# Performance work log

Hardware: AMD Instinct MI355X
Metric: run time of the kernel (lower is better)

## Reference

```python
import jax, jax.numpy as jnp
import numpy as np

EPS = 1e-12  # matches torch F.normalize eps


def setup_inputs() -> dict:
    key = jax.random.key(0)
    k1, k2 = jax.random.split(key)
    N, D, K = 262144, 128, 512
    embeddings = jax.random.normal(k1, (N, D), dtype=jnp.float32)
    init_centroids = jax.random.normal(k2, (K, D), dtype=jnp.float32)
    return {"embeddings": embeddings, "init_centroids": init_centroids, "num_iters": 5}


def _kmeans_iter(centroids, embeddings, K):
    # [N, K] similarity, hard assignment by argmax (k-means E-step with dot-product metric)
    dots = jnp.matmul(embeddings, centroids.T)
    assign = jnp.argmax(dots, axis=1)  # [N] int32
    # M-step: per-cluster sum + counts (replaces CPU dict-of-lists + python loop)
    emb_sums = jax.ops.segment_sum(embeddings, assign, num_segments=K)  # [K, D]
    counts = jax.ops.segment_sum(jnp.ones(embeddings.shape[0], dtype=embeddings.dtype),
                                 assign, num_segments=K)  # [K]
    # only update clusters with members (mask = counts > 0), keep old centroid otherwise
    new_c = jnp.where(counts[:, None] > 0,
                      emb_sums / jnp.maximum(counts, 1.0)[:, None],
                      centroids)
    # F.normalize(dim=1, p=2) applied to ALL centroids
    norm = jnp.maximum(jnp.linalg.norm(new_c, axis=1, keepdims=True), EPS)
    return new_c / norm, assign


def reference(embeddings, init_centroids, num_iters):
    K = init_centroids.shape[0]
    centroids = init_centroids
    assign = jnp.zeros(embeddings.shape[0], dtype=jnp.int32)
    for _ in range(num_iters):  # small static iteration count (k-means iters)
        centroids, assign = _kmeans_iter(centroids, embeddings, K)
    return assign, centroids
```

## Files before the change

### kernel.cpp

```cpp
#include <hip/hip_runtime.h>

#define NN 262144
#define DD 128
#define KK 512
#define NITER 5

#define SKH 136

#define SE 132
#define SC 260
#define SS 129

#define DELTA 2e-3f

#define WS_A16_BYTES   (NN * 2)
#define WS_SUMS_OFF    (WS_A16_BYTES)
#define WS_CNTS_OFF    (WS_SUMS_OFF + 2048 * DD * 4)
#define WS_NEEDED      (WS_CNTS_OFF + 2048 * 4)
#define WS_CH_OFF      (WS_SUMS_OFF + NN)
#define WS_CL_OFF      (WS_CH_OFF + KK * DD * 2)
#define WS_EAB3_OFF    (WS_NEEDED)
#define WS_EAB3_BYTES  (NN * DD * 4)
#define WS_NEEDED2     (WS_EAB3_OFF + WS_EAB3_BYTES)

using s8     = __attribute__((ext_vector_type(8))) short;
using f32x4  = __attribute__((ext_vector_type(4))) float;
using f32x16 = __attribute__((ext_vector_type(16))) float;

__device__ __forceinline__ unsigned f2bf(float x) {
    unsigned u = __float_as_uint(x);
    return (u + 0x7fffu + ((u >> 16) & 1u)) >> 16;
}

__device__ __forceinline__ void split4(float4 v, uint2& h, uint2& s) {
    unsigned hx = f2bf(v.x), hy = f2bf(v.y), hz = f2bf(v.z), hw = f2bf(v.w);
    float rx = v.x - __uint_as_float(hx << 16);
    float ry = v.y - __uint_as_float(hy << 16);
    float rz = v.z - __uint_as_float(hz << 16);
    float rw = v.w - __uint_as_float(hw << 16);
    unsigned lx = f2bf(rx), ly = f2bf(ry), lz = f2bf(rz), lw = f2bf(rw);
    h.x = hx | (hy << 16); h.y = hz | (hw << 16);
    s.x = lx | (ly << 16); s.y = lz | (lw << 16);
}

__global__ __launch_bounds__(256) void presplit_e3_kernel(
    const float* __restrict__ E, unsigned short* __restrict__ EAB)
{
    const int u   = blockIdx.x * 4 + (threadIdx.x >> 6);
    const int l   = threadIdx.x & 63;
    const int g32 = u >> 3, ks = u & 7;
    const int row = g32 * 32 + (l & 31);
    const int k0  = ks * 16 + (l >> 5) * 8;
    float4 v0 = *(const float4*)&E[(size_t)row * DD + k0];
    float4 v1 = *(const float4*)&E[(size_t)row * DD + k0 + 4];
    uint2 h0, s0, h1, s1;
    split4(v0, h0, s0); split4(v1, h1, s1);
    size_t base = (size_t)u * 2048 + l * 16;
    *(uint2*)((char*)EAB + base)        = h0;
    *(uint2*)((char*)EAB + base + 8)    = h1;
    *(uint2*)((char*)EAB + base + 1024) = s0;
    *(uint2*)((char*)EAB + base + 1032) = s1;
}

__global__ __launch_bounds__(256) void split_c3_kernel(
    const float* __restrict__ C, unsigned short* __restrict__ CH,
    unsigned short* __restrict__ CL)
{
    int idx = blockIdx.x * 256 + threadIdx.x;
    int col = idx >> 5;
    int k4  = (idx & 31) << 2;
    float4 v = *(const float4*)&C[(size_t)col * DD + k4];
    uint2 h, s;
    split4(v, h, s);
    int unit = (col >> 5) * 8 + (k4 >> 4);
    int lane = (col & 31) + ((k4 >> 3) & 1) * 32;
    int off  = unit * 512 + lane * 8 + (k4 & 7);
    *(uint2*)&CH[off] = h;
    *(uint2*)&CL[off] = s;
}

__global__ __launch_bounds__(256, 2) void assign4_kernel(
    const unsigned short* __restrict__ EAB,
    const unsigned short* __restrict__ CH, const unsigned short* __restrict__ CL,
    int* __restrict__ assignv, unsigned short* __restrict__ assign16,
    unsigned char* __restrict__ flags)
{
    const int tid = threadIdx.x;
    const int l   = tid & 63;
    const int wid = tid >> 6;
    const int j   = l & 31;
    const int h   = l >> 5;
    const int r0  = blockIdx.x * 128;
    const int g32 = blockIdx.x * 4 + wid;

    const char* Abase = (const char*)EAB + (size_t)g32 * 16384 + l * 16;
    s8 Ah[8], Al[8];
#pragma unroll
    for (int ks = 0; ks < 8; ++ks) {
        Ah[ks] = *(const s8*)(Abase + ks * 2048);
        Al[ks] = *(const s8*)(Abase + ks * 2048 + 1024);
    }

    float bv[16], sv[16];
    int   bk[16];
#pragma unroll
    for (int i = 0; i < 16; ++i) { bv[i] = -3.4e38f; sv[i] = -3.4e38f; bk[i] = 0; }

    const int boff0 = l * 8;

    s8 bh[2][4], bl[2][4];
#pragma unroll
    for (int cf = 0; cf < 4; ++cf) {
        bh[0][cf] = *(const s8*)&CH[(cf * 8) * 512 + boff0];
        bl[0][cf] = *(const s8*)&CL[(cf * 8) * 512 + boff0];
    }

    f32x16 acc[4];

#pragma unroll
    for (int t = 0; t < 32; ++t) {
        const int cc  = t >> 3, ks = t & 7;
        const int cur = t & 1,  nxt = cur ^ 1;

        if (ks == 0) {
#pragma unroll
            for (int cf = 0; cf < 4; ++cf)
#pragma unroll
                for (int r = 0; r < 16; ++r) acc[cf][r] = 0.f;
        }

        if (t < 31) {
            const int t1 = t + 1, cc1 = t1 >> 3, ks1 = t1 & 7;
#pragma unroll
            for (int cf = 0; cf < 4; ++cf) {
                const int unit = (cc1 * 4 + cf) * 8 + ks1;
                bh[nxt][cf] = *(const s8*)&CH[unit * 512 + boff0];
                bl[nxt][cf] = *(const s8*)&CL[unit * 512 + boff0];
            }
        }

#pragma unroll
        for (int cf = 0; cf < 4; ++cf) {
            acc[cf] = __builtin_amdgcn_mfma_f32_32x32x16_bf16(
                Ah[ks], bh[cur][cf], acc[cf], 0, 0, 0);
            acc[cf] = __builtin_amdgcn_mfma_f32_32x32x16_bf16(
                Ah[ks], bl[cur][cf], acc[cf], 0, 0, 0);
            acc[cf] = __builtin_amdgcn_mfma_f32_32x32x16_bf16(
                Al[ks], bh[cur][cf], acc[cf], 0, 0, 0);
        }

        if (ks == 7) {
#pragma unroll
            for (int cf = 0; cf < 4; ++cf) {
                const int kg = cc * 128 + cf * 32 + j;
#pragma unroll
                for (int r = 0; r < 16; ++r) {
                    float v = acc[cf][r];
                    if (v > bv[r]) { sv[r] = bv[r]; bv[r] = v; bk[r] = kg; }
                    else           { sv[r] = fmaxf(sv[r], v); }
                }
            }
        }
    }

#pragma unroll
    for (int r = 0; r < 16; ++r) {
        float v1 = bv[r], v2 = sv[r]; int k1 = bk[r];
#pragma unroll
        for (int m = 1; m <= 16; m <<= 1) {
            float ov = __shfl_xor(v1, m, 64);
            float os = __shfl_xor(v2, m, 64);
            int   ok = __shfl_xor(k1, m, 64);
            if (ov > v1) { v2 = fmaxf(v1, os); v1 = ov; k1 = ok; }
            else         { v2 = fmaxf(v2, ov); }
        }
        bv[r] = v1; sv[r] = v2; bk[r] = k1;
    }

#pragma unroll
    for (int r = 0; r < 16; ++r) {
        if (j == r) {
            int rowg = r0 + wid * 32 + (r & 3) + 8 * (r >> 2) + 4 * h;
            assignv[rowg]  = bk[r];
            assign16[rowg] = (unsigned short)bk[r];
            flags[rowg]    = (bv[r] - sv[r] < DELTA) ? 1 : 0;
        }
    }
}

__global__ __launch_bounds__(256) void split_c_kernel(
    const float* __restrict__ C, unsigned short* __restrict__ CH,
    unsigned short* __restrict__ CL)
{
    int idx = blockIdx.x * 256 + threadIdx.x;
    int col = idx >> 5;
    int k4  = (idx & 31) << 2;
    float4 v = *(const float4*)&C[(size_t)col * DD + k4];
    uint2 h, s;
    split4(v, h, s);
    int group = (col >> 4) * 4 + (k4 >> 5);
    int inner = ((k4 >> 3) & 3) * 16 + (col & 15);
    int off   = group * 512 + inner * 8 + (k4 & 7);
    *(uint2*)&CH[off] = h;
    *(uint2*)&CL[off] = s;
}

__global__ __launch_bounds__(256, 2) void assign_kernel(
    const float* __restrict__ E,
    const unsigned short* __restrict__ CH, const unsigned short* __restrict__ CL,
    int* __restrict__ assignv, unsigned short* __restrict__ assign16,
    unsigned char* __restrict__ flags)
{
    __shared__ unsigned short lds[2 * 128 * SKH];
    unsigned short* EH = lds;
    unsigned short* EL = lds + 128 * SKH;

    const int tid = threadIdx.x;
    const int l   = tid & 63;
    const int wid = tid >> 6;
    const int wr  = wid >> 1;
    const int wc  = wid & 1;
    const int c   = l & 15;
    const int g   = l >> 4;
    const int r0  = blockIdx.x * 128;

#pragma unroll
    for (int it = 0; it < 16; ++it) {
        int idx = it * 256 + tid;
        int row = idx >> 5;
        int k4  = (idx & 31) << 2;
        float4 v = *(const float4*)&E[(size_t)(r0 + row) * DD + k4];
        uint2 h, s;
        split4(v, h, s);
        *(uint2*)&EH[row * SKH + k4] = h;
        *(uint2*)&EL[row * SKH + k4] = s;
    }
    __syncthreads();

    float bv[16], sv[16];
    int   bk[16];
#pragma unroll
    for (int i = 0; i < 16; ++i) { bv[i] = -3.4e38f; sv[i] = -3.4e38f; bk[i] = 0; }

    const int aoff0 = (wr * 64 + c) * SKH + g * 8;
    const int bbase = wc * 16 * 512 + l * 8;

    s8 bh[2][4], bl[2][4];
#pragma unroll
    for (int cf = 0; cf < 4; ++cf) {
        int off = bbase + (cf * 4) * 512;
        bh[0][cf] = *(const s8*)&CH[off];
        bl[0][cf] = *(const s8*)&CL[off];
    }

    f32x4 acc[4][4];

#pragma unroll
    for (int t = 0; t < 16; ++t) {
        const int cc  = t >> 2, kc = t & 3;
        const int cur = t & 1,  nxt = cur ^ 1;

        if (kc == 0) {
#pragma unroll
            for (int rf = 0; rf < 4; ++rf)
#pragma unroll
                for (int cf = 0; cf < 4; ++cf)
                    acc[rf][cf] = (f32x4){0.f, 0.f, 0.f, 0.f};
        }

        if (t < 15) {
            const int t1 = t + 1, cc1 = t1 >> 2, kc1 = t1 & 3;
#pragma unroll
            for (int cf = 0; cf < 4; ++cf) {
                int off = bbase + (cc1 * 32 + cf * 4 + kc1) * 512;
                bh[nxt][cf] = *(const s8*)&CH[off];
                bl[nxt][cf] = *(const s8*)&CL[off];
            }
        }

        s8 ah[4], al[4];
#pragma unroll
        for (int rf = 0; rf < 4; ++rf) {
            int off = aoff0 + rf * 16 * SKH + kc * 32;
            ah[rf] = *(const s8*)&EH[off];
            al[rf] = *(const s8*)&EL[off];
        }

#pragma unroll
        for (int rf = 0; rf < 4; ++rf)
#pragma unroll
            for (int cf = 0; cf < 4; ++cf) {
                acc[rf][cf] = __builtin_amdgcn_mfma_f32_16x16x32_bf16(
                    ah[rf], bh[cur][cf], acc[rf][cf], 0, 0, 0);
                acc[rf][cf] = __builtin_amdgcn_mfma_f32_16x16x32_bf16(
                    ah[rf], bl[cur][cf], acc[rf][cf], 0, 0, 0);
                acc[rf][cf] = __builtin_amdgcn_mfma_f32_16x16x32_bf16(
                    al[rf], bh[cur][cf], acc[rf][cf], 0, 0, 0);
            }

        if (kc == 3) {
            const int kbase = cc * 128 + wc * 64 + c;
#pragma unroll
            for (int rf = 0; rf < 4; ++rf)
#pragma unroll
                for (int i = 0; i < 4; ++i) {
                    const int sidx = rf * 4 + i;
#pragma unroll
                    for (int cf = 0; cf < 4; ++cf) {
                        float v = acc[rf][cf][i];
                        int  kg = kbase + cf * 16;
                        if (v > bv[sidx]) { sv[sidx] = bv[sidx]; bv[sidx] = v; bk[sidx] = kg; }
                        else              { sv[sidx] = fmaxf(sv[sidx], v); }
                    }
                }
        }
    }

#pragma unroll
    for (int s = 0; s < 16; ++s) {
        float v1 = bv[s], v2 = sv[s]; int k1 = bk[s];
#pragma unroll
        for (int m = 1; m <= 8; m <<= 1) {
            float ov = __shfl_xor(v1, m, 64);
            float os = __shfl_xor(v2, m, 64);
            int   ok = __shfl_xor(k1, m, 64);
            if (ov > v1) { v2 = fmaxf(v1, os); v1 = ov; k1 = ok; }
            else         { v2 = fmaxf(v2, ov); }
        }
        bv[s] = v1; sv[s] = v2; bk[s] = k1;
    }

    __syncthreads();
    float* mv = (float*)lds;
    int*   mk = (int*)lds + 256;
    float* ms = (float*)lds + 512;
    if (c == 0) {
#pragma unroll
        for (int rf = 0; rf < 4; ++rf)
#pragma unroll
            for (int i = 0; i < 4; ++i) {
                int row = wr * 64 + rf * 16 + g * 4 + i;
                mv[wc * 128 + row] = bv[rf * 4 + i];
                mk[wc * 128 + row] = bk[rf * 4 + i];
                ms[wc * 128 + row] = sv[rf * 4 + i];
            }
    }
    __syncthreads();
    if (tid < 128) {
        float v1 = mv[tid], v2 = ms[tid]; int k1 = mk[tid];
        float ov = mv[128 + tid], os = ms[128 + tid]; int ok = mk[128 + tid];
        if (ov > v1) { v2 = fmaxf(v1, os); v1 = ov; k1 = ok; }
        else         { v2 = fmaxf(v2, ov); }
        assignv[r0 + tid] = k1;
        assign16[r0 + tid] = (unsigned short)k1;
        flags[r0 + tid] = (v1 - v2 < DELTA) ? 1 : 0;
    }
}

__global__ __launch_bounds__(256) void rescue_kernel(
    const float* __restrict__ E, const float* __restrict__ C,
    const unsigned char* __restrict__ flags,
    int* __restrict__ assignv, unsigned short* __restrict__ assign16)
{
    __shared__ int   rows[128];
    __shared__ int   nf;
    __shared__ float ev[DD];
    __shared__ float rv[4];
    __shared__ int   rk[4];

    const int tid  = threadIdx.x;
    const int base = blockIdx.x * 128;

    if (tid == 0) nf = 0;
    __syncthreads();
    if (tid < 128 && flags[base + tid]) {
        int p = atomicAdd(&nf, 1);
        rows[p] = base + tid;
    }
    __syncthreads();
    const int n = nf;
    if (n == 0) return;

    for (int i = 0; i < n; ++i) {
        const int row = rows[i];
        if (tid < 32)
            *(float4*)&ev[tid * 4] = *(const float4*)&E[(size_t)row * DD + tid * 4];
        __syncthreads();

        float d0 = 0.f, d1 = 0.f;
        for (int q = 0; q < 32; ++q) {
            float4 e4 = *(const float4*)&ev[q * 4];
            float4 c0 = *(const float4*)&C[(size_t)tid * DD + q * 4];
            float4 c1 = *(const float4*)&C[(size_t)(tid + 256) * DD + q * 4];
            d0 = fmaf(e4.x, c0.x, d0); d0 = fmaf(e4.y, c0.y, d0);
            d0 = fmaf(e4.z, c0.z, d0); d0 = fmaf(e4.w, c0.w, d0);
            d1 = fmaf(e4.x, c1.x, d1); d1 = fmaf(e4.y, c1.y, d1);
            d1 = fmaf(e4.z, c1.z, d1); d1 = fmaf(e4.w, c1.w, d1);
        }
        float v = (d0 >= d1) ? d0 : d1;
        int   k = (d0 >= d1) ? tid : tid + 256;
#pragma unroll
        for (int m = 1; m <= 32; m <<= 1) {
            float ov = __shfl_xor(v, m, 64);
            int   ok = __shfl_xor(k, m, 64);
            if (ov > v || (ov == v && ok < k)) { v = ov; k = ok; }
        }
        if ((tid & 63) == 0) { rv[tid >> 6] = v; rk[tid >> 6] = k; }
        __syncthreads();
        if (tid == 0) {
            float bv2 = rv[0]; int bk2 = rk[0];
#pragma unroll
            for (int w = 1; w < 4; ++w)
                if (rv[w] > bv2 || (rv[w] == bv2 && rk[w] < bk2)) { bv2 = rv[w]; bk2 = rk[w]; }
            assignv[row] = bk2;
            assign16[row] = (unsigned short)bk2;
        }
        __syncthreads();
    }
}

__global__ __launch_bounds__(256, 2) void assign_valu_kernel(
    const float* __restrict__ E, const float* __restrict__ C,
    int* __restrict__ assignv, unsigned short* __restrict__ assign16)
{
    __shared__ float smem[32 * SE + 32 * SC];
    float* ET = smem;
    float* CT = smem + 32 * SE;
    float* sval = smem;
    int*   sidx = ((int*)smem) + 32 * SS;

    const int tid = threadIdx.x;
    const int tx  = tid & 31;
    const int ty  = tid >> 5;
    const int r0  = blockIdx.x * 128;

    float bbv = 0.f;
    int   bbk = 0;

    for (int chunk = 0; chunk < 2; ++chunk) {
        const int k0 = chunk * 256;
        float acc[16][8];
#pragma unroll
        for (int i = 0; i < 16; ++i)
#pragma unroll
            for (int j = 0; j < 8; ++j) acc[i][j] = 0.f;

        for (int sub = 0; sub < 4; ++sub) {
            const int d0 = sub * 32;
            __syncthreads();
#pragma unroll
            for (int it = 0; it < 4; ++it) {
                int idx = tid + it * 256;
                int r = idx >> 3, q = idx & 7;
                float4 v = *(const float4*)&E[(r0 + r) * DD + d0 + q * 4];
                ET[(q * 4 + 0) * SE + r] = v.x;
                ET[(q * 4 + 1) * SE + r] = v.y;
                ET[(q * 4 + 2) * SE + r] = v.z;
                ET[(q * 4 + 3) * SE + r] = v.w;
            }
#pragma unroll
            for (int it = 0; it < 8; ++it) {
                int idx = tid + it * 256;
                int k = idx >> 3, q = idx & 7;
                float4 v = *(const float4*)&C[(k0 + k) * DD + d0 + q * 4];
                CT[(q * 4 + 0) * SC + k] = v.x;
                CT[(q * 4 + 1) * SC + k] = v.y;
                CT[(q * 4 + 2) * SC + k] = v.z;
                CT[(q * 4 + 3) * SC + k] = v.w;
            }
            __syncthreads();
#pragma unroll 4
            for (int d = 0; d < 32; ++d) {
                float4 a0 = *(const float4*)&ET[d * SE + ty * 16];
                float4 a1 = *(const float4*)&ET[d * SE + ty * 16 + 4];
                float4 a2 = *(const float4*)&ET[d * SE + ty * 16 + 8];
                float4 a3 = *(const float4*)&ET[d * SE + ty * 16 + 12];
                float4 b0 = *(const float4*)&CT[d * SC + tx * 4];
                float4 b1 = *(const float4*)&CT[d * SC + 128 + tx * 4];
                float ra[16] = {a0.x, a0.y, a0.z, a0.w, a1.x, a1.y, a1.z, a1.w,
                                a2.x, a2.y, a2.z, a2.w, a3.x, a3.y, a3.z, a3.w};
                float rb[8]  = {b0.x, b0.y, b0.z, b0.w, b1.x, b1.y, b1.z, b1.w};
#pragma unroll
                for (int i = 0; i < 16; ++i)
#pragma unroll
                    for (int j = 0; j < 8; ++j)
                        acc[i][j] = fmaf(ra[i], rb[j], acc[i][j]);
            }
        }
        __syncthreads();

#pragma unroll
        for (int i = 0; i < 16; ++i) {
            float bv = acc[i][0]; int bj = 0;
#pragma unroll
            for (int j = 1; j < 8; ++j)
                if (acc[i][j] > bv) { bv = acc[i][j]; bj = j; }
            int row = ty * 16 + i;
            int gk = k0 + ((bj < 4) ? (tx * 4 + bj) : (128 + tx * 4 + (bj - 4)));
            sval[tx * SS + row] = bv;
            sidx[tx * SS + row] = gk;
        }
        __syncthreads();
        if (tid < 128) {
            float bv = sval[tid]; int bi = sidx[tid];
            for (int t = 1; t < 32; ++t) {
                float v = sval[t * SS + tid];
                int   x = sidx[t * SS + tid];
                if (v > bv || (v == bv && x < bi)) { bv = v; bi = x; }
            }
            if (chunk == 0 || bv > bbv || (bv == bbv && bi < bbk)) {
                bbv = bv; bbk = bi;
            }
        }
    }
    if (tid < 128) {
        assignv[r0 + tid] = bbk;
        if (assign16) assign16[r0 + tid] = (unsigned short)bbk;
    }
}

__global__ __launch_bounds__(256) void update_partial_kernel(
    const float* __restrict__ E, const unsigned short* __restrict__ assign16,
    float* __restrict__ ws_sums, int* __restrict__ ws_cnts)
{
    const int b   = blockIdx.x;
    const int k   = b >> 2;
    const int qtr = b & 3;

    __shared__ float acc[4][DD];
    __shared__ int   cnts[4];

    const int tid  = threadIdx.x;
    const int w    = tid >> 6;
    const int lane = tid & 63;

    float a0 = 0.f, a1 = 0.f;
    int cnt = 0;
    const int wbase = qtr * (NN / 4) + w * (NN / 16);

    for (int it = 0; it < (NN / 16) / 512; ++it) {
        const int off = wbase + it * 512;
        uint4 p = *(const uint4*)&assign16[off + lane * 8];
        unsigned v[4] = {p.x, p.y, p.z, p.w};
#pragma unroll
        for (int h = 0; h < 4; ++h) {
            int lo = (int)(v[h] & 0xffffu);
            int hi = (int)(v[h] >> 16);
            unsigned long long mlo = __ballot(lo == k);
            unsigned long long mhi = __ballot(hi == k);
            cnt += (int)__popcll(mlo) + (int)__popcll(mhi);
            while (mlo) {
                int b2 = __ffsll((long long)mlo) - 1; mlo &= mlo - 1;
                int row = off + b2 * 8 + h * 2;
                float2 e = *(const float2*)&E[(size_t)row * DD + lane * 2];
                a0 += e.x; a1 += e.y;
            }
            while (mhi) {
                int b2 = __ffsll((long long)mhi) - 1; mhi &= mhi - 1;
                int row = off + b2 * 8 + h * 2 + 1;
                float2 e = *(const float2*)&E[(size_t)row * DD + lane * 2];
                a0 += e.x; a1 += e.y;
            }
        }
    }
    acc[w][lane * 2]     = a0;
    acc[w][lane * 2 + 1] = a1;
    if (lane == 0) cnts[w] = cnt;
    __syncthreads();
    if (tid < DD)
        ws_sums[(size_t)b * DD + tid] = acc[0][tid] + acc[1][tid] + acc[2][tid] + acc[3][tid];
    if (tid == 0)
        ws_cnts[b] = cnts[0] + cnts[1] + cnts[2] + cnts[3];
}

__global__ __launch_bounds__(128) void update_combine_kernel(
    const float* __restrict__ ws_sums, const int* __restrict__ ws_cnts,
    float* __restrict__ C)
{
    const int k = blockIdx.x, t = threadIdx.x;
    __shared__ float red[2];
    const int w = t >> 6, lane = t & 63;

    float s = ws_sums[(size_t)(4 * k + 0) * DD + t]
            + ws_sums[(size_t)(4 * k + 1) * DD + t]
            + ws_sums[(size_t)(4 * k + 2) * DD + t]
            + ws_sums[(size_t)(4 * k + 3) * DD + t];
    int cnt = ws_cnts[4 * k] + ws_cnts[4 * k + 1] + ws_cnts[4 * k + 2] + ws_cnts[4 * k + 3];
    float m = (cnt > 0) ? s / (float)cnt : C[k * DD + t];

    float sq = m * m;
#pragma unroll
    for (int o = 32; o > 0; o >>= 1) sq += __shfl_down(sq, o, 64);
    if (lane == 0) red[w] = sq;
    __syncthreads();
    float nrm = fmaxf(sqrtf(red[0] + red[1]), 1e-12f);
    C[k * DD + t] = m / nrm;
}

__global__ __launch_bounds__(256) void update_kernel(
    const float* __restrict__ E, const int* __restrict__ assignv,
    float* __restrict__ C)
{
    const int k = blockIdx.x;
    __shared__ float acc[4][DD];
    __shared__ int   cnts[4];
    __shared__ float red[4];

    const int tid  = threadIdx.x;
    const int w    = tid >> 6;
    const int lane = tid & 63;

    float a0 = 0.f, a1 = 0.f;
    int cnt = 0;
    const int per_wave = NN / 4;
    const int base = w * per_wave;

    for (int it = 0; it < per_wave / 256; ++it) {
        const int off = base + it * 256;
        int4 as = *(const int4*)&assignv[off + lane * 4];
        int av[4] = {as.x, as.y, as.z, as.w};
#pragma unroll
        for (int ci = 0; ci < 4; ++ci) {
            unsigned long long m = __ballot(av[ci] == k);
            cnt += (int)__popcll(m);
            while (m) {
                int b = __ffsll((long long)m) - 1;
                m &= m - 1;
                int r = off + b * 4 + ci;
                float2 v = *(const float2*)&E[r * DD + lane * 2];
                a0 += v.x; a1 += v.y;
            }
        }
    }
    acc[w][lane * 2]     = a0;
    acc[w][lane * 2 + 1] = a1;
    if (lane == 0) cnts[w] = cnt;
    __syncthreads();

    float m = 0.f;
    const int ctot = cnts[0] + cnts[1] + cnts[2] + cnts[3];
    if (tid < DD) {
        float s = acc[0][tid] + acc[1][tid] + acc[2][tid] + acc[3][tid];
        m = (ctot > 0) ? s / (float)ctot : C[k * DD + tid];
    }
    float sq = m * m;
#pragma unroll
    for (int o = 32; o > 0; o >>= 1) sq += __shfl_down(sq, o, 64);
    if (lane == 0) red[w] = sq;
    __syncthreads();
    if (tid < DD) {
        float nrm = fmaxf(sqrtf(red[0] + red[1]), 1e-12f);
        C[k * DD + tid] = m / nrm;
    }
}

__global__ void finalize_kernel(float* __restrict__ out)
{
    int i = blockIdx.x * 256 + threadIdx.x;
    if (i < NN) {
        int a = ((const int*)out)[i];
        out[i] = (float)a;
    }
}

extern "C" void kernel_launch(void* const* d_in, const int* in_sizes, int n_in,
                              void* d_out, int out_size, void* d_ws, size_t ws_size,
                              hipStream_t stream)
{
    (void)in_sizes; (void)n_in; (void)out_size;

    const float* E  = (const float*)d_in[0];
    const float* C0 = (const float*)d_in[1];

    float* out     = (float*)d_out;
    float* C       = out + NN;
    int*   assignv = (int*)out;

    const bool fast  = (ws_size >= (size_t)WS_NEEDED);
    const bool fast2 = (ws_size >= (size_t)WS_NEEDED2);
    unsigned short* assign16 = fast ? (unsigned short*)d_ws : nullptr;
    float* ws_sums = fast ? (float*)((char*)d_ws + WS_SUMS_OFF) : nullptr;
    int*   ws_cnts = fast ? (int*)((char*)d_ws + WS_CNTS_OFF) : nullptr;
    unsigned char* flags = fast ? (unsigned char*)d_ws + WS_SUMS_OFF : nullptr;
    unsigned short* CH = fast ? (unsigned short*)((char*)d_ws + WS_CH_OFF) : nullptr;
    unsigned short* CL = fast ? (unsigned short*)((char*)d_ws + WS_CL_OFF) : nullptr;
    unsigned short* EAB = fast2 ? (unsigned short*)((char*)d_ws + WS_EAB3_OFF) : nullptr;

    hipMemcpyAsync(C, C0, (size_t)KK * DD * sizeof(float),
                   hipMemcpyDeviceToDevice, stream);

    if (fast2)
        presplit_e3_kernel<<<16384, 256, 0, stream>>>(E, EAB);

    for (int it = 0; it < NITER; ++it) {
        if (fast2) {
            split_c3_kernel<<<KK * DD / 4 / 256, 256, 0, stream>>>(C, CH, CL);
            assign4_kernel<<<NN / 128, 256, 0, stream>>>(EAB, CH, CL,
                                                         assignv, assign16, flags);
            rescue_kernel<<<NN / 128, 256, 0, stream>>>(E, C, flags, assignv, assign16);
            update_partial_kernel<<<2048, 256, 0, stream>>>(E, assign16, ws_sums, ws_cnts);
            update_combine_kernel<<<KK, 128, 0, stream>>>(ws_sums, ws_cnts, C);
        } else if (fast) {
            split_c_kernel<<<KK * DD / 4 / 256, 256, 0, stream>>>(C, CH, CL);
            assign_kernel<<<NN / 128, 256, 0, stream>>>(E, CH, CL, assignv, assign16, flags);
            rescue_kernel<<<NN / 128, 256, 0, stream>>>(E, C, flags, assignv, assign16);
            update_partial_kernel<<<2048, 256, 0, stream>>>(E, assign16, ws_sums, ws_cnts);
            update_combine_kernel<<<KK, 128, 0, stream>>>(ws_sums, ws_cnts, C);
        } else {
            assign_valu_kernel<<<NN / 128, 256, 0, stream>>>(E, C, assignv, nullptr);
            update_kernel<<<KK, 256, 0, stream>>>(E, assignv, C);
        }
    }
    finalize_kernel<<<(NN + 255) / 256, 256, 0, stream>>>(out);
}
```

Baseline: 1.371 ms.

## Stage centroid tiles through double-buffered LDS in assign kernel

The assign kernel now loads centroid hi/lo bf16 tiles cooperatively into a 64KB double-buffered shared-memory area, and each wave reads its MFMA B operands from LDS. Before, every wave fetched B fragments directly from global memory. Centroids are processed in eight chunks of 64, with register prefetch of the next chunk overlapped with MFMA work. This cuts redundant global and L2 traffic across the four waves, at the cost of 64KB of LDS per block, which may limit occupancy against the requested two blocks per CU, plus a block barrier per chunk.

After: 1.253 ms. -8.6%, faster.

```diff
diff --git a/kernel.cpp b/kernel.cpp
--- a/kernel.cpp
+++ b/kernel.cpp
@@ -79,12 +79,14 @@
     *(uint2*)&CL[off] = s;
 }
 
-__global__ __launch_bounds__(256, 2) void assign4_kernel(
+__global__ __launch_bounds__(256, 2) void assign5_kernel(
     const unsigned short* __restrict__ EAB,
     const unsigned short* __restrict__ CH, const unsigned short* __restrict__ CL,
     int* __restrict__ assignv, unsigned short* __restrict__ assign16,
     unsigned char* __restrict__ flags)
 {
+    __shared__ char bld[2][32768];
+
     const int tid = threadIdx.x;
     const int l   = tid & 63;
     const int wid = tid >> 6;
@@ -106,60 +108,76 @@
 #pragma unroll
     for (int i = 0; i < 16; ++i) { bv[i] = -3.4e38f; sv[i] = -3.4e38f; bk[i] = 0; }
 
-    const int boff0 = l * 8;
-
-    s8 bh[2][4], bl[2][4];
-#pragma unroll
-    for (int cf = 0; cf < 4; ++cf) {
-        bh[0][cf] = *(const s8*)&CH[(cf * 8) * 512 + boff0];
-        bl[0][cf] = *(const s8*)&CL[(cf * 8) * 512 + boff0];
-    }
-
-    f32x16 acc[4];
-
-#pragma unroll
-    for (int t = 0; t < 32; ++t) {
-        const int cc  = t >> 3, ks = t & 7;
-        const int cur = t & 1,  nxt = cur ^ 1;
-
-        if (ks == 0) {
-#pragma unroll
-            for (int cf = 0; cf < 4; ++cf)
-#pragma unroll
-                for (int r = 0; r < 16; ++r) acc[cf][r] = 0.f;
-        }
-
-        if (t < 31) {
-            const int t1 = t + 1, cc1 = t1 >> 3, ks1 = t1 & 7;
-#pragma unroll
-            for (int cf = 0; cf < 4; ++cf) {
-                const int unit = (cc1 * 4 + cf) * 8 + ks1;
-                bh[nxt][cf] = *(const s8*)&CH[unit * 512 + boff0];
-                bl[nxt][cf] = *(const s8*)&CL[unit * 512 + boff0];
-            }
-        }
-
-#pragma unroll
-        for (int cf = 0; cf < 4; ++cf) {
-            acc[cf] = __builtin_amdgcn_mfma_f32_32x32x16_bf16(
-                Ah[ks], bh[cur][cf], acc[cf], 0, 0, 0);
-            acc[cf] = __builtin_amdgcn_mfma_f32_32x32x16_bf16(
-                Ah[ks], bl[cur][cf], acc[cf], 0, 0, 0);
-            acc[cf] = __builtin_amdgcn_mfma_f32_32x32x16_bf16(
-                Al[ks], bh[cur][cf], acc[cf], 0, 0, 0);
-        }
-
-        if (ks == 7) {
-#pragma unroll
-            for (int cf = 0; cf < 4; ++cf) {
-                const int kg = cc * 128 + cf * 32 + j;
-#pragma unroll
-                for (int r = 0; r < 16; ++r) {
-                    float v = acc[cf][r];
-                    if (v > bv[r]) { sv[r] = bv[r]; bv[r] = v; bk[r] = kg; }
-                    else           { sv[r] = fmaxf(sv[r], v); }
-                }
-            }
+    {
+        uint4 rH[4], rL[4];
+#pragma unroll
+        for (int p = 0; p < 4; ++p) {
+            rH[p] = *(const uint4*)((const char*)CH + (p * 256 + tid) * 16);
+            rL[p] = *(const uint4*)((const char*)CL + (p * 256 + tid) * 16);
+        }
+#pragma unroll
+        for (int p = 0; p < 4; ++p) {
+            *(uint4*)(bld[0] + (p * 256 + tid) * 16)         = rH[p];
+            *(uint4*)(bld[0] + 16384 + (p * 256 + tid) * 16) = rL[p];
+        }
+    }
+    __syncthreads();
+
+#pragma unroll
+    for (int hc = 0; hc < 8; ++hc) {
+        const int cur = hc & 1, nxt = cur ^ 1;
+
+        uint4 rH[4], rL[4];
+        if (hc < 7) {
+            const char* srcH = (const char*)CH + (hc + 1) * 16384;
+            const char* srcL = (const char*)CL + (hc + 1) * 16384;
+#pragma unroll
+            for (int p = 0; p < 4; ++p) {
+                rH[p] = *(const uint4*)(srcH + (p * 256 + tid) * 16);
+                rL[p] = *(const uint4*)(srcL + (p * 256 + tid) * 16);
+            }
+        }
+
+        f32x16 acc[2];
+#pragma unroll
+        for (int cfi = 0; cfi < 2; ++cfi)
+#pragma unroll
+            for (int r = 0; r < 16; ++r) acc[cfi][r] = 0.f;
+
+#pragma unroll
+        for (int ks = 0; ks < 8; ++ks) {
+#pragma unroll
+            for (int cfi = 0; cfi < 2; ++cfi) {
+                const int uu = cfi * 8 + ks;
+                s8 bh = *(const s8*)(bld[cur] + uu * 1024 + l * 16);
+                s8 bl = *(const s8*)(bld[cur] + 16384 + uu * 1024 + l * 16);
+                acc[cfi] = __builtin_amdgcn_mfma_f32_32x32x16_bf16(
+                    Ah[ks], bh, acc[cfi], 0, 0, 0);
+                acc[cfi] = __builtin_amdgcn_mfma_f32_32x32x16_bf16(
+                    Ah[ks], bl, acc[cfi], 0, 0, 0);
+                acc[cfi] = __builtin_amdgcn_mfma_f32_32x32x16_bf16(
+                    Al[ks], bh, acc[cfi], 0, 0, 0);
+            }
+        }
+
+#pragma unroll
+        for (int cfi = 0; cfi < 2; ++cfi) {
+            const int kg = hc * 64 + cfi * 32 + j;
+#pragma unroll
+            for (int r = 0; r < 16; ++r) {
+                float v = acc[cfi][r];
+                if (v > bv[r]) { sv[r] = bv[r]; bv[r] = v; bk[r] = kg; }
+                else           { sv[r] = fmaxf(sv[r], v); }
+            }
+        }
+
+        if (hc < 7) {
+#pragma unroll
+            for (int p = 0; p < 4; ++p) {
+                *(uint4*)(bld[nxt] + (p * 256 + tid) * 16)         = rH[p];
+                *(uint4*)(bld[nxt] + 16384 + (p * 256 + tid) * 16) = rL[p];
+            }
+            __syncthreads();
         }
     }
 
@@ -695,7 +713,7 @@
     for (int it = 0; it < NITER; ++it) {
         if (fast2) {
             split_c3_kernel<<<KK * DD / 4 / 256, 256, 0, stream>>>(C, CH, CL);
-            assign4_kernel<<<NN / 128, 256, 0, stream>>>(EAB, CH, CL,
+            assign5_kernel<<<NN / 128, 256, 0, stream>>>(EAB, CH, CL,
                                                          assignv, assign16, flags);
             rescue_kernel<<<NN / 128, 256, 0, stream>>>(E, C, flags, assignv, assign16);
             update_partial_kernel<<<2048, 256, 0, stream>>>(E, assign16, ws_sums, ws_cnts);
```
